# Optimization experiments

Measured on AMD Instinct MI355X. Metric: run time of the kernel, lower is better.

The kernel has to match this reference:

```python
import jax, jax.numpy as jnp
import numpy as np

NEG = -1e4      # BigBird additive mask value
LN_EPS = 1e-12  # BERT-style LayerNorm eps


def _bigbird_forward(xs_pad, mask, Wq, bq, Wk, bk, Wv, bv, Wo, bo, gamma, beta, rand_idx):
    b, n, hsz = xs_pad.shape
    H = rand_idx.shape[0]
    nb = rand_idx.shape[1] + 2          # one rand row per non-edge query block
    BS = n // nb                        # block size
    d = hsz // H
    r = rand_idx.shape[2]
    scale = 1.0 / np.sqrt(d).astype(np.float32)

    mf = mask.reshape(b, n).astype(xs_pad.dtype)   # (b,n) 1=token, 0=pad
    mb = mf.reshape(b, nb, BS)                     # blocked mask

    def proj(W, bias):
        return (xs_pad @ W + bias).reshape(b, n, H, d).transpose(0, 2, 1, 3)

    q = proj(Wq, bq) * scale            # (b,H,n,d)
    k = proj(Wk, bk)
    v = proj(Wv, bv)
    qb = q.reshape(b, H, nb, BS, d)
    kb = k.reshape(b, H, nb, BS, d)
    vb = v.reshape(b, H, nb, BS, d)

    # ---- global rows: first / last query block attend to all keys ----
    def full_row(qi):                   # qi: (b,H,BS,d)
        s = jnp.einsum('bhqd,bhkd->bhqk', qi, k) + (1.0 - mf)[:, None, None, :] * NEG
        return jnp.einsum('bhqk,bhkd->bhqd', jax.nn.softmax(s, axis=-1), v)

    ctx_first = full_row(qb[:, :, 0])
    ctx_last = full_row(qb[:, :, nb - 1])

    # ---- random key/value blocks: per-head, per-query-block gather ----
    hidx = jnp.arange(H)[:, None, None]
    rand_k = kb[:, hidx, rand_idx].reshape(b, H, nb - 2, r * BS, d)
    rand_v = vb[:, hidx, rand_idx].reshape(b, H, nb - 2, r * BS, d)
    rand_m = mb[:, rand_idx].reshape(b, H, nb - 2, r * BS)

    def sparse_row(qi, kc, vc, mc):     # kc:(b,H,K,d), mc:(b,H,K)
        s = jnp.einsum('bhqd,bhkd->bhqk', qi, kc) + (1.0 - mc)[:, :, None, :] * NEG
        return jnp.einsum('bhqk,bhkd->bhqd', jax.nn.softmax(s, axis=-1), vc)

    def gather_blocks(ids, ridx):
        kc = jnp.concatenate([kb[:, :, j] for j in ids] + [rand_k[:, :, ridx]], axis=2)
        vc = jnp.concatenate([vb[:, :, j] for j in ids] + [rand_v[:, :, ridx]], axis=2)
        mc = jnp.concatenate([jnp.broadcast_to(mb[:, None, j], (b, H, BS)) for j in ids]
                             + [rand_m[:, :, ridx]], axis=2)
        return kc, vc, mc

    # second / penultimate query blocks: window + globals + rand
    ctx_second = sparse_row(qb[:, :, 1], *gather_blocks([0, 1, 2, nb - 1], 0))
    ctx_penult = sparse_row(qb[:, :, nb - 2], *gather_blocks([nb - 3, nb - 2, nb - 1, 0], nb - 3))

    # ---- middle rows i in [2, nb-3]: 3-block sliding window + first/last global + r random ----
    nmid = nb - 4
    mid = jnp.arange(2, nb - 2)
    win = mid[:, None] + jnp.arange(-1, 2)[None, :]        # (nmid,3)
    k_win = kb[:, :, win].reshape(b, H, nmid, 3 * BS, d)
    v_win = vb[:, :, win].reshape(b, H, nmid, 3 * BS, d)
    m_win = jnp.broadcast_to(mb[:, win].reshape(b, 1, nmid, 3 * BS), (b, H, nmid, 3 * BS))

    def rep_glob(t):                     # (b,H,BS,...) -> (b,H,nmid,BS,...)
        return jnp.broadcast_to(t[:, :, None], (b, H, nmid) + t.shape[2:])

    k_mid = jnp.concatenate([k_win, rep_glob(kb[:, :, 0]), rep_glob(kb[:, :, nb - 1]),
                             rand_k[:, :, 1:nb - 3]], axis=3)
    v_mid = jnp.concatenate([v_win, rep_glob(vb[:, :, 0]), rep_glob(vb[:, :, nb - 1]),
                             rand_v[:, :, 1:nb - 3]], axis=3)
    m_first = jnp.broadcast_to(mb[:, None, None, 0], (b, H, nmid, BS))
    m_last = jnp.broadcast_to(mb[:, None, None, nb - 1], (b, H, nmid, BS))
    m_mid = jnp.concatenate([m_win, m_first, m_last, rand_m[:, :, 1:nb - 3]], axis=3)

    s_mid = jnp.einsum('bhmqd,bhmkd->bhmqk', qb[:, :, 2:nb - 2], k_mid) \
            + (1.0 - m_mid)[:, :, :, None, :] * NEG
    ctx_mid = jnp.einsum('bhmqk,bhmkd->bhmqd', jax.nn.softmax(s_mid, axis=-1), v_mid)

    ctx = jnp.concatenate([ctx_first[:, :, None], ctx_second[:, :, None], ctx_mid,
                           ctx_penult[:, :, None], ctx_last[:, :, None]], axis=2)
    ctx = ctx.reshape(b, H, n, d).transpose(0, 2, 1, 3).reshape(b, n, hsz)
    ctx = ctx * mf[:, :, None]           # from_mask on output rows

    # BigBirdSelfOutput: dense + residual + LayerNorm (dropout=0 / eval)
    y = ctx @ Wo + bo + xs_pad
    mu = y.mean(-1, keepdims=True)
    var = ((y - mu) ** 2).mean(-1, keepdims=True)
    return (y - mu) * jax.lax.rsqrt(var + LN_EPS) * gamma + beta


def setup_inputs() -> dict:
    key = jax.random.key(0)
    ks = jax.random.split(key, 6)
    B, N, HSZ, H, BS, R = 4, 4096, 1024, 16, 64, 3
    NB = N // BS
    init = lambda k, shp: jax.random.normal(k, shp, dtype=jnp.float32) * 0.02
    return {
        'xs_pad': jax.random.normal(ks[0], (B, N, HSZ), dtype=jnp.float32),
        'mask': jnp.ones((B, 1, N), dtype=jnp.int32),
        'Wq': init(ks[1], (HSZ, HSZ)), 'bq': jnp.zeros((HSZ,), jnp.float32),
        'Wk': init(ks[2], (HSZ, HSZ)), 'bk': jnp.zeros((HSZ,), jnp.float32),
        'Wv': init(ks[3], (HSZ, HSZ)), 'bv': jnp.zeros((HSZ,), jnp.float32),
        'Wo': init(ks[4], (HSZ, HSZ)), 'bo': jnp.zeros((HSZ,), jnp.float32),
        'gamma': jnp.ones((HSZ,), jnp.float32), 'beta': jnp.zeros((HSZ,), jnp.float32),
        'rand_idx': jax.random.randint(ks[5], (H, NB - 2, R), 1, NB - 1).astype(jnp.int32),
    }


def reference(xs_pad, mask, Wq, bq, Wk, bk, Wv, bv, Wo, bo, gamma, beta, rand_idx):
    return _bigbird_forward(xs_pad, mask, Wq, bq, Wk, bk, Wv, bv, Wo, bo, gamma, beta, rand_idx)
```

## Files before the change

kernel.cpp:

```cpp
#include <hip/hip_runtime.h>
#include <hip/hip_bf16.h>

#define B_   4
#define N_   4096
#define HSZ  1024
#define H_   16
#define D_   64
#define NB_  64
#define R_   3
#define M_   (B_*N_)
#define NEGV (-1e4f)
#define LOG2E 1.4426950408889634f

typedef float f32x4 __attribute__((ext_vector_type(4)));
typedef short s16x8 __attribute__((ext_vector_type(8)));
typedef __bf16 b16x8 __attribute__((ext_vector_type(8)));

__device__ __forceinline__ f32x4 mfma16(s16x8 a, s16x8 b, f32x4 c) {
  return __builtin_amdgcn_mfma_f32_16x16x32_bf16(
      __builtin_bit_cast(b16x8, a), __builtin_bit_cast(b16x8, b), c, 0, 0, 0);
}

__device__ __forceinline__ short f2b(float x) {
  __hip_bfloat16 h = __float2bfloat16(x);
  return (short)__builtin_bit_cast(unsigned short, h);
}

__device__ __forceinline__ unsigned pack2(float a, float b) {
  return (unsigned)(unsigned short)f2b(a) |
         ((unsigned)(unsigned short)f2b(b) << 16);
}

__device__ __forceinline__ void gl_lds16(const short* g, short* l) {
  __builtin_amdgcn_global_load_lds(
      (const __attribute__((address_space(1))) unsigned int*)g,
      (__attribute__((address_space(3))) unsigned int*)l, 16, 0, 0);
}

__global__ __launch_bounds__(256) void k_prep(const float* __restrict__ in,
                                              short* __restrict__ out,
                                              const float* __restrict__ Wq,
                                              const float* __restrict__ Wk,
                                              const float* __restrict__ Wv,
                                              const float* __restrict__ Wo,
                                              short* __restrict__ wt) {
  const int tid = threadIdx.x;
  if (blockIdx.x < 8192) {
    size_t i = ((size_t)blockIdx.x * 256 + tid) * 8;
    float4 a = *(const float4*)&in[i];
    float4 b = *(const float4*)&in[i + 4];
    s16x8 o;
    o[0] = f2b(a.x); o[1] = f2b(a.y); o[2] = f2b(a.z); o[3] = f2b(a.w);
    o[4] = f2b(b.x); o[5] = f2b(b.y); o[6] = f2b(b.z); o[7] = f2b(b.w);
    *(s16x8*)&out[i] = o;
    return;
  }
  const int bid = blockIdx.x - 8192;
  const int z = bid >> 8;
  const int rest = bid & 255;
  const int tk = (rest >> 4) * 64, tn = (rest & 15) * 64;
  const float* src = (z == 0) ? Wq : (z == 1) ? Wk : (z == 2) ? Wv : Wo;
  short* dst = wt + (size_t)z * HSZ * HSZ;
  __shared__ __align__(16) float t[64][68];
#pragma unroll
  for (int r = 0; r < 4; ++r) {
    int c = tid + r * 256;
    int row = c >> 4, seg = c & 15;
    *(float4*)&t[row][seg * 4] =
        *(const float4*)&src[(size_t)(tk + row) * HSZ + tn + seg * 4];
  }
  __syncthreads();
#pragma unroll
  for (int r = 0; r < 2; ++r) {
    int c = tid + r * 256;
    int row = c >> 3, seg = c & 7;
    s16x8 o;
#pragma unroll
    for (int u = 0; u < 8; ++u) o[u] = f2b(t[seg * 8 + u][row]);
    *(s16x8*)&dst[(size_t)(tn + row) * HSZ + tk + seg * 8] = o;
  }
}

template <bool SWAP>
__device__ __forceinline__ void gemm8_core(
    const short* __restrict__ A, const short* __restrict__ Bt, int tm, int tn,
    short (&a_lds)[2][256][64], short (&b_lds)[2][256][64],
    f32x4 (&acc)[8][4], int wave, int lane) {
  const int lq = lane & 15, g = lane >> 4;
  const int wm = wave >> 2, wn = wave & 3;
  const int sl8 = lane >> 3;
  const int sc = ((lane & 7) ^ sl8) * 8;

  auto ST_A = [&](int buf, int kt, int h) {
#pragma unroll
    for (int u = 0; u < 2; ++u) {
      const int rbase = h * 128 + wave * 8 + u * 64;
      gl_lds16(&A[(size_t)(tm + rbase + sl8) * HSZ + kt * 64 + sc],
               &a_lds[buf][rbase][0]);
    }
  };
  auto ST_B = [&](int buf, int kt, int h) {
#pragma unroll
    for (int u = 0; u < 2; ++u) {
      const int rbase = h * 128 + wave * 8 + u * 64;
      gl_lds16(&Bt[(size_t)(tn + rbase + sl8) * HSZ + kt * 64 + sc],
               &b_lds[buf][rbase][0]);
    }
  };

  s16x8 bf[4][2];
  auto LOADB = [&](int buf) {
#pragma unroll
    for (int j = 0; j < 4; ++j) {
      const int row = wn * 64 + j * 16 + lq;
#pragma unroll
      for (int kk = 0; kk < 2; ++kk)
        bf[j][kk] =
            *(const s16x8*)&b_lds[buf][row][((kk * 4 + g) ^ (lq & 7)) * 8];
    }
  };
  auto PH = [&](int buf, int m0) {
    s16x8 af[2][2];
#pragma unroll
    for (int i = 0; i < 2; ++i) {
      const int row = wm * 128 + (m0 + i) * 16 + lq;
#pragma unroll
      for (int kk = 0; kk < 2; ++kk)
        af[i][kk] =
            *(const s16x8*)&a_lds[buf][row][((kk * 4 + g) ^ (lq & 7)) * 8];
    }
    __builtin_amdgcn_s_setprio(1);
#pragma unroll
    for (int i = 0; i < 2; ++i)
#pragma unroll
      for (int j = 0; j < 4; ++j)
#pragma unroll
        for (int kk = 0; kk < 2; ++kk)
          acc[m0 + i][j] = SWAP
                               ? mfma16(bf[j][kk], af[i][kk], acc[m0 + i][j])
                               : mfma16(af[i][kk], bf[j][kk], acc[m0 + i][j]);
    __builtin_amdgcn_s_setprio(0);
    __builtin_amdgcn_s_barrier();
  };

  ST_A(0, 0, 0); ST_A(0, 0, 1);
  ST_B(0, 0, 0); ST_B(0, 0, 1);
  ST_B(1, 1, 0); ST_B(1, 1, 1);

  for (int p = 0; p < 8; ++p) {
    const int t = 2 * p;
    ST_A(1, t + 1, 0); ST_A(1, t + 1, 1);
    asm volatile("s_waitcnt vmcnt(8)" ::: "memory");
    __builtin_amdgcn_s_barrier();
    LOADB(0);
    PH(0, 0);
    if (t + 2 < 16) { ST_B(0, t + 2, 0); ST_B(0, t + 2, 1); }
    PH(0, 2);
    PH(0, 4);
    PH(0, 6);
    if (t + 2 < 16) { ST_A(0, t + 2, 0); ST_A(0, t + 2, 1); }
    if (p < 7) {
      asm volatile("s_waitcnt vmcnt(8)" ::: "memory");
    } else {
      asm volatile("s_waitcnt vmcnt(0)" ::: "memory");
    }
    __builtin_amdgcn_s_barrier();
    LOADB(1);
    PH(1, 0);
    if (t + 3 < 16) { ST_B(1, t + 3, 0); ST_B(1, t + 3, 1); }
    PH(1, 2);
    PH(1, 4);
    PH(1, 6);
  }
}

__global__ __launch_bounds__(512, 2) void k_qkv(
    const short* __restrict__ A, const short* __restrict__ WT,
    const float* __restrict__ bq, const float* __restrict__ bk,
    const float* __restrict__ bv, short* __restrict__ oq,
    short* __restrict__ ok, short* __restrict__ ovt) {
  const int orig = blockIdx.x;
  const int xcd = orig & 7, r = orig >> 3;
  const int tml = r / 12, rem = r % 12;
  const int z = rem >> 2, tnl = rem & 3;
  const int tm = (xcd * 8 + tml) * 256, tn = tnl * 256;
  const short* Bt = WT + (size_t)z * HSZ * HSZ;

  __shared__ __align__(16) short a_lds[2][256][64];
  __shared__ __align__(16) short b_lds[2][256][64];

  const int tid = threadIdx.x, lane = tid & 63, wave = tid >> 6;
  const int lq = lane & 15, g = lane >> 4;
  const int wm = wave >> 2, wn = wave & 3;

  f32x4 acc[8][4] = {};

  if (z == 2) {
    gemm8_core<false>(A, Bt, tm, tn, a_lds, b_lds, acc, wave, lane);
#pragma unroll
    for (int j = 0; j < 4; ++j) {
      const int col = tn + wn * 64 + j * 16 + lq;
      const int hh = col >> 6, dd = col & 63;
      const float bi = bv[col];
#pragma unroll
      for (int i = 0; i < 8; ++i) {
        const int nrow = tm + wm * 128 + i * 16 + g * 4;
        const int bb = nrow >> 12, nn = nrow & (N_ - 1);
        uint2 w;
        w.x = pack2(acc[i][j][0] + bi, acc[i][j][1] + bi);
        w.y = pack2(acc[i][j][2] + bi, acc[i][j][3] + bi);
        *(uint2*)&ovt[(((size_t)bb * H_ + hh) * D_ + dd) * N_ + nn] = w;
      }
    }
  } else {
    gemm8_core<true>(A, Bt, tm, tn, a_lds, b_lds, acc, wave, lane);
    const float* bias = z ? bk : bq;
    short* outb = z ? ok : oq;
    const float alpha = z ? 1.0f : 0.125f * LOG2E;
#pragma unroll
    for (int i = 0; i < 8; ++i) {
      const int row = tm + wm * 128 + i * 16 + lq;
#pragma unroll
      for (int j = 0; j < 4; ++j) {
        const int colb = tn + wn * 64 + j * 16 + g * 4;
        const float4 bi = *(const float4*)&bias[colb];
        const int bb = row >> 12, nn = row & (N_ - 1);
        const int hh = colb >> 6, dd = colb & 63;
        uint2 w;
        w.x = pack2((acc[i][j][0] + bi.x) * alpha,
                    (acc[i][j][1] + bi.y) * alpha);
        w.y = pack2((acc[i][j][2] + bi.z) * alpha,
                    (acc[i][j][3] + bi.w) * alpha);
        *(uint2*)&outb[(((size_t)bb * H_ + hh) * N_ + nn) * D_ + dd] = w;
      }
    }
  }
}

__global__ __launch_bounds__(512, 2) void k_out(
    const short* __restrict__ A, const short* __restrict__ WT,
    const float* __restrict__ bo, const float* __restrict__ xs,
    float* __restrict__ yout) {
  const short* Bt = WT + (size_t)3 * HSZ * HSZ;

  __shared__ __align__(16) short a_lds[2][256][64];
  __shared__ __align__(16) short b_lds[2][256][64];

  const int tid = threadIdx.x, lane = tid & 63, wave = tid >> 6;
  const int lq = lane & 15, g = lane >> 4;
  const int wm = wave >> 2, wn = wave & 3;
  const int orig = blockIdx.x;
  const int xcd = orig & 7, r = orig >> 3;
  const int tml = r >> 2, tnl = r & 3;
  const int tm = (xcd * 8 + tml) * 256, tn = tnl * 256;

  f32x4 acc[8][4] = {};
  gemm8_core<true>(A, Bt, tm, tn, a_lds, b_lds, acc, wave, lane);

#pragma unroll
  for (int i = 0; i < 8; ++i) {
    const int row = tm + wm * 128 + i * 16 + lq;
#pragma unroll
    for (int j = 0; j < 4; ++j) {
      const int colb = tn + wn * 64 + j * 16 + g * 4;
      const float4 bi = *(const float4*)&bo[colb];
      const size_t idx = (size_t)row * HSZ + colb;
      const float4 xv = *(const float4*)&xs[idx];
      float4 yv;
      yv.x = acc[i][j][0] + bi.x + xv.x;
      yv.y = acc[i][j][1] + bi.y + xv.y;
      yv.z = acc[i][j][2] + bi.z + xv.z;
      yv.w = acc[i][j][3] + bi.w + xv.w;
      *(float4*)&yout[idx] = yv;
    }
  }
}

__global__ __launch_bounds__(256) void k_attn(
    const short* __restrict__ Q, const short* __restrict__ K,
    const short* __restrict__ VT, const int* __restrict__ mask,
    const int* __restrict__ rnd, short* __restrict__ ctx,
    float* __restrict__ pO, float* __restrict__ pm, float* __restrict__ pl) {
  const int orig = blockIdx.x;
  const int swg = (orig & 7) * 624 + (orig >> 3);
  const int s = swg % 78;
  const int bh_i = swg / 78;
  const int h = bh_i & 15, b = bh_i >> 4;
  const int tid = threadIdx.x, lane = tid & 63, wave = tid >> 6;
  const int g = lane >> 4, lq = lane & 15;

  __shared__ __align__(16) short k_lds[64][64];
  __shared__ __align__(16) short vt_lds[64][64];
  __shared__ __align__(16) short p_lds[4][16][72];
  __shared__ __align__(16) float bias_s[8][64];
  __shared__ int list_s[8];
  __shared__ int Ls;

  const bool mid = (s < 62);
  const int qb = mid ? (s + 1) : (((s - 62) >> 3) ? (NB_ - 1) : 0);

  if (tid == 0) {
    int L;
    if (!mid) {
      int chunk = (s - 62) & 7;
#pragma unroll
      for (int i = 0; i < 8; ++i) list_s[i] = chunk * 8 + i;
      L = 8;
    } else {
      const int* rp = rnd + ((size_t)h * (NB_ - 2) + (qb - 1)) * R_;
      int n;
      if (qb == 1) {
        list_s[0] = 0; list_s[1] = 1; list_s[2] = 2; list_s[3] = NB_ - 1; n = 4;
      } else if (qb == NB_ - 2) {
        list_s[0] = NB_ - 3; list_s[1] = NB_ - 2; list_s[2] = NB_ - 1;
        list_s[3] = 0; n = 4;
      } else {
        list_s[0] = qb - 1; list_s[1] = qb; list_s[2] = qb + 1;
        list_s[3] = 0; list_s[4] = NB_ - 1; n = 5;
      }
      for (int j = 0; j < R_; ++j) list_s[n + j] = rp[j];
      L = n + R_;
      for (int i = L; i < 8; ++i) list_s[i] = 0;
    }
    Ls = L;
  }

  const size_t bh = (size_t)b * H_ + h;
  const size_t qrow = bh * N_ + (size_t)qb * 64 + wave * 16 + lq;
  s16x8 qf0 = *(const s16x8*)&Q[qrow * D_ + g * 8];
  s16x8 qf1 = *(const s16x8*)&Q[qrow * D_ + 32 + g * 8];

  __syncthreads();
  const int L = Ls;

  const int r0 = tid >> 3, sg = tid & 7;
  const int csl = (sg ^ (r0 & 7)) * 8;
  const int sw = (lq & 7);

  const short* Kb = K + bh * (size_t)N_ * D_;
  const short* Vb = VT + bh * (size_t)D_ * N_;
  const int* mb = mask + (size_t)b * N_;

  for (int t = tid; t < 512; t += 256) {
    const int i = t >> 6, kk2 = t & 63;
    bias_s[i][kk2] =
        (1.0f - (float)mb[list_s[i] * 64 + kk2]) * (NEGV * LOG2E);
  }

  s16x8 kr0, kr1, vr0, vr1;
  {
    const int kb = list_s[0];
    const short* kp = Kb + (size_t)kb * 64 * D_;
    const short* vp = Vb + (size_t)kb * 64;
    kr0 = *(const s16x8*)&kp[(size_t)r0 * D_ + sg * 8];
    kr1 = *(const s16x8*)&kp[(size_t)(r0 + 32) * D_ + sg * 8];
    vr0 = *(const s16x8*)&vp[(size_t)r0 * N_ + sg * 8];
    vr1 = *(const s16x8*)&vp[(size_t)(r0 + 32) * N_ + sg * 8];
  }

  s16x8 ones;
#pragma unroll
  for (int u = 0; u < 8; ++u) ones[u] = (short)0x3F80;

  f32x4 o[4] = {};
  f32x4 osum = {};
  float mshift = 0.0f;

  for (int it = 0; it < L; ++it) {
    *(s16x8*)&k_lds[r0][csl] = kr0;
    *(s16x8*)&k_lds[r0 + 32][csl] = kr1;
    *(s16x8*)&vt_lds[r0][csl] = vr0;
    *(s16x8*)&vt_lds[r0 + 32][csl] = vr1;
    if (it + 1 < L) {
      const int kb = list_s[it + 1];
      const short* kp = Kb + (size_t)kb * 64 * D_;
      const short* vp = Vb + (size_t)kb * 64;
      kr0 = *(const s16x8*)&kp[(size_t)r0 * D_ + sg * 8];
      kr1 = *(const s16x8*)&kp[(size_t)(r0 + 32) * D_ + sg * 8];
      vr0 = *(const s16x8*)&vp[(size_t)r0 * N_ + sg * 8];
      vr1 = *(const s16x8*)&vp[(size_t)(r0 + 32) * N_ + sg * 8];
    }
    __syncthreads();

    f32x4 st[4];
#pragma unroll
    for (int f = 0; f < 4; ++f) {
      f32x4 a0 = *(const f32x4*)&bias_s[it][f * 16 + g * 4];
      s16x8 af0 = *(const s16x8*)&k_lds[f * 16 + lq][(g ^ sw) * 8];
      s16x8 af1 = *(const s16x8*)&k_lds[f * 16 + lq][((4 + g) ^ sw) * 8];
      a0 = mfma16(af0, qf0, a0);
      a0 = mfma16(af1, qf1, a0);
      st[f] = a0;
    }

    if (mshift == 0.0f) {
#pragma unroll
      for (int f = 0; f < 4; ++f)
#pragma unroll
        for (int e = 0; e < 4; ++e) st[f][e] = exp2f(st[f][e]);
    } else {
#pragma unroll
      for (int f = 0; f < 4; ++f)
#pragma unroll
        for (int e = 0; e < 4; ++e) st[f][e] = exp2f(st[f][e] - mshift);
    }

#pragma unroll
    for (int f = 0; f < 4; ++f) {
      uint2 w = make_uint2(pack2(st[f][0], st[f][1]),
                           pack2(st[f][2], st[f][3]));
      *(uint2*)&p_lds[wave][lq][f * 16 + g * 4] = w;
    }

#pragma unroll
    for (int kk = 0; kk < 2; ++kk) {
      s16x8 pa = *(const s16x8*)&p_lds[wave][lq][kk * 32 + g * 8];
#pragma unroll
      for (int j = 0; j < 4; ++j) {
        s16x8 bv =
            *(const s16x8*)&vt_lds[j * 16 + lq][((kk * 4 + g) ^ sw) * 8];
        o[j] = mfma16(pa, bv, o[j]);
      }
      osum = mfma16(pa, ones, osum);
    }

    float om = fmaxf(fmaxf(osum[0], osum[1]), fmaxf(osum[2], osum[3]));
    if (__any(om > 16777216.0f)) {
#pragma unroll
      for (int j = 0; j < 4; ++j) o[j] *= 5.9604645e-08f;
      osum *= 5.9604645e-08f;
      mshift += 24.0f;
    }
    __syncthreads();
  }

  if (mid) {
    float rs[4];
#pragma unroll
    for (int e = 0; e < 4; ++e)
      rs[e] = (float)mb[qb * 64 + wave * 16 + g * 4 + e] /
              fmaxf(osum[e], 1e-30f);
#pragma unroll
    for (int j = 0; j < 4; ++j) {
      k_lds[wave * 16 + g * 4 + 0][j * 16 + lq] = f2b(o[j][0] * rs[0]);
      k_lds[wave * 16 + g * 4 + 1][j * 16 + lq] = f2b(o[j][1] * rs[1]);
      k_lds[wave * 16 + g * 4 + 2][j * 16 + lq] = f2b(o[j][2] * rs[2]);
      k_lds[wave * 16 + g * 4 + 3][j * 16 + lq] = f2b(o[j][3] * rs[3]);
    }
    __syncthreads();
#pragma unroll
    for (int pp = 0; pp < 2; ++pp) {
      int c = tid + pp * 256;
      int row = c >> 3, seg = c & 7;
      *(s16x8*)&ctx[((size_t)b * N_ + qb * 64 + row) * HSZ + h * D_ + seg * 8] =
          *(const s16x8*)&k_lds[row][seg * 8];
    }
  } else {
    const int e2 = s - 62;
    const int qsel = e2 >> 3, chunk = e2 & 7;
    const size_t eidx = (bh * 2 + qsel) * 8 + chunk;
    float* po = pO + eidx * 4096;
#pragma unroll
    for (int j = 0; j < 4; ++j)
#pragma unroll
      for (int e = 0; e < 4; ++e)
        po[(wave * 16 + g * 4 + e) * 64 + j * 16 + lq] = o[j][e];
    if (lq == 0) {
#pragma unroll
      for (int e = 0; e < 4; ++e) {
        pm[eidx * 64 + wave * 16 + g * 4 + e] = mshift;
        pl[eidx * 64 + wave * 16 + g * 4 + e] = osum[e];
      }
    }
  }
}

__global__ __launch_bounds__(256) void k_comb(
    const float* __restrict__ pO, const float* __restrict__ pm,
    const float* __restrict__ pl, const int* __restrict__ mask,
    short* __restrict__ ctx) {
  const int qsel = blockIdx.x, h = blockIdx.y, b = blockIdx.z;
  const int qb = qsel ? NB_ - 1 : 0;
  const int tid = threadIdx.x;
  const int q = tid >> 2, dq = tid & 3;
  const size_t base = (((size_t)b * H_ + h) * 2 + qsel) * 8;

  float mv[8];
  float M = -INFINITY;
#pragma unroll
  for (int i = 0; i < 8; ++i) {
    mv[i] = pm[(base + i) * 64 + q];
    M = fmaxf(M, mv[i]);
  }
  float Lsum = 0.0f;
#pragma unroll
  for (int i = 0; i < 8; ++i) {
    float w = exp2f(mv[i] - M);
    mv[i] = w;
    Lsum += pl[(base + i) * 64 + q] * w;
  }
  f32x4 acc[4] = {};
#pragma unroll
  for (int i = 0; i < 8; ++i) {
    const float* p = pO + (base + i) * 4096 + q * 64 + dq * 16;
    float w = mv[i];
#pragma unroll
    for (int u = 0; u < 4; ++u) {
      f32x4 v = *(const f32x4*)&p[u * 4];
      acc[u] += v * w;
    }
  }
  float sc = (float)mask[(size_t)b * N_ + qb * 64 + q] / fmaxf(Lsum, 1e-30f);
  s16x8 out0, out1;
#pragma unroll
  for (int u = 0; u < 8; ++u) {
    out0[u] = f2b(acc[u >> 2][u & 3] * sc);
    out1[u] = f2b(acc[2 + (u >> 2)][u & 3] * sc);
  }
  short* dst = &ctx[((size_t)b * N_ + qb * 64 + q) * HSZ + h * D_ + dq * 16];
  *(s16x8*)dst = out0;
  *(s16x8*)(dst + 8) = out1;
}

__global__ __launch_bounds__(256) void k_ln(float* __restrict__ y,
                                            const float* __restrict__ gamma,
                                            const float* __restrict__ beta) {
  const int row = blockIdx.x, tid = threadIdx.x, lane = tid & 63,
            wave = tid >> 6;
  __shared__ float s_sum[4], s_sq[4];
  float4 v = *(const float4*)&y[(size_t)row * HSZ + tid * 4];
  float s = v.x + v.y + v.z + v.w;
  float q = v.x * v.x + v.y * v.y + v.z * v.z + v.w * v.w;
#pragma unroll
  for (int m = 1; m <= 32; m <<= 1) {
    s += __shfl_xor(s, m);
    q += __shfl_xor(q, m);
  }
  if (lane == 0) { s_sum[wave] = s; s_sq[wave] = q; }
  __syncthreads();
  float S = s_sum[0] + s_sum[1] + s_sum[2] + s_sum[3];
  float Qs = s_sq[0] + s_sq[1] + s_sq[2] + s_sq[3];
  float mu = S * (1.0f / HSZ);
  float var = Qs * (1.0f / HSZ) - mu * mu;
  float r = rsqrtf(var + 1e-12f);
  float4 g = *(const float4*)&gamma[tid * 4];
  float4 be = *(const float4*)&beta[tid * 4];
  float4 outv;
  outv.x = (v.x - mu) * r * g.x + be.x;
  outv.y = (v.y - mu) * r * g.y + be.y;
  outv.z = (v.z - mu) * r * g.z + be.z;
  outv.w = (v.w - mu) * r * g.w + be.w;
  *(float4*)&y[(size_t)row * HSZ + tid * 4] = outv;
}

extern "C" void kernel_launch(void* const* d_in, const int* in_sizes, int n_in,
                              void* d_out, int out_size, void* d_ws,
                              size_t ws_size, hipStream_t stream) {
  const float* xs = (const float*)d_in[0];
  const int* mask = (const int*)d_in[1];
  const float* Wq = (const float*)d_in[2];
  const float* bq = (const float*)d_in[3];
  const float* Wk = (const float*)d_in[4];
  const float* bk = (const float*)d_in[5];
  const float* Wv = (const float*)d_in[6];
  const float* bv = (const float*)d_in[7];
  const float* Wo = (const float*)d_in[8];
  const float* bo = (const float*)d_in[9];
  const float* gamma = (const float*)d_in[10];
  const float* beta = (const float*)d_in[11];
  const int* rnd = (const int*)d_in[12];
  float* yout = (float*)d_out;

  char* ws = (char*)d_ws;
  const size_t SZ_XS = (size_t)M_ * HSZ * 2;
  const size_t SZ_WT = (size_t)4 * HSZ * HSZ * 2;
  short* xsb = (short*)ws;
  short* wt = (short*)(ws + SZ_XS);
  short* qbuf = (short*)(ws + SZ_XS + SZ_WT);
  short* kbuf = qbuf + (size_t)M_ * HSZ;
  short* vtb = kbuf + (size_t)M_ * HSZ;
  char* after = ws + SZ_XS + SZ_WT + 3 * SZ_XS;
  float* pO = (float*)(after + (1 << 20));
  float* pm = pO + (size_t)1024 * 4096;
  float* pl = pm + (size_t)1024 * 64;

  k_prep<<<9216, 256, 0, stream>>>(xs, xsb, Wq, Wk, Wv, Wo, wt);
  k_qkv<<<768, 512, 0, stream>>>(xsb, wt, bq, bk, bv, qbuf, kbuf, vtb);
  k_attn<<<4992, 256, 0, stream>>>(qbuf, kbuf, vtb, mask, rnd, xsb, pO, pm,
                                   pl);
  k_comb<<<dim3(2, H_, B_), 256, 0, stream>>>(pO, pm, pl, mask, xsb);
  k_out<<<256, 512, 0, stream>>>(xsb, wt, bo, xs, yout);
  k_ln<<<M_, 256, 0, stream>>>(yout, gamma, beta);
}
```

Before: 325.4 us.

## Double-buffer K/V tiles in attention and relax GEMM launch bounds

The attention kernel now keeps two LDS buffers for the K and V^T tiles, alternating by iteration parity. This lets it drop the trailing barrier in each key-block loop iteration, leaving one barrier per iteration instead of two. A barrier is added before the output staging that reuses buffer 0. The two GEMM kernels also drop the min-2-blocks-per-CU hint from their launch bounds, giving the compiler more register freedom at the possible cost of occupancy.

```diff
diff --git a/kernel.cpp b/kernel.cpp
--- a/kernel.cpp
+++ b/kernel.cpp
@@ -174,7 +174,7 @@
   }
 }
 
-__global__ __launch_bounds__(512, 2) void k_qkv(
+__global__ __launch_bounds__(512) void k_qkv(
     const short* __restrict__ A, const short* __restrict__ WT,
     const float* __restrict__ bq, const float* __restrict__ bk,
     const float* __restrict__ bv, short* __restrict__ oq,
@@ -237,7 +237,7 @@
   }
 }
 
-__global__ __launch_bounds__(512, 2) void k_out(
+__global__ __launch_bounds__(512) void k_out(
     const short* __restrict__ A, const short* __restrict__ WT,
     const float* __restrict__ bo, const float* __restrict__ xs,
     float* __restrict__ yout) {
@@ -289,8 +289,8 @@
   const int tid = threadIdx.x, lane = tid & 63, wave = tid >> 6;
   const int g = lane >> 4, lq = lane & 15;
 
-  __shared__ __align__(16) short k_lds[64][64];
-  __shared__ __align__(16) short vt_lds[64][64];
+  __shared__ __align__(16) short k_lds[2][64][64];
+  __shared__ __align__(16) short vt_lds[2][64][64];
   __shared__ __align__(16) short p_lds[4][16][72];
   __shared__ __align__(16) float bias_s[8][64];
   __shared__ int list_s[8];
@@ -367,10 +367,11 @@
   float mshift = 0.0f;
 
   for (int it = 0; it < L; ++it) {
-    *(s16x8*)&k_lds[r0][csl] = kr0;
-    *(s16x8*)&k_lds[r0 + 32][csl] = kr1;
-    *(s16x8*)&vt_lds[r0][csl] = vr0;
-    *(s16x8*)&vt_lds[r0 + 32][csl] = vr1;
+    const int buf = it & 1;
+    *(s16x8*)&k_lds[buf][r0][csl] = kr0;
+    *(s16x8*)&k_lds[buf][r0 + 32][csl] = kr1;
+    *(s16x8*)&vt_lds[buf][r0][csl] = vr0;
+    *(s16x8*)&vt_lds[buf][r0 + 32][csl] = vr1;
     if (it + 1 < L) {
       const int kb = list_s[it + 1];
       const short* kp = Kb + (size_t)kb * 64 * D_;
@@ -386,8 +387,8 @@
 #pragma unroll
     for (int f = 0; f < 4; ++f) {
       f32x4 a0 = *(const f32x4*)&bias_s[it][f * 16 + g * 4];
-      s16x8 af0 = *(const s16x8*)&k_lds[f * 16 + lq][(g ^ sw) * 8];
-      s16x8 af1 = *(const s16x8*)&k_lds[f * 16 + lq][((4 + g) ^ sw) * 8];
+      s16x8 af0 = *(const s16x8*)&k_lds[buf][f * 16 + lq][(g ^ sw) * 8];
+      s16x8 af1 = *(const s16x8*)&k_lds[buf][f * 16 + lq][((4 + g) ^ sw) * 8];
       a0 = mfma16(af0, qf0, a0);
       a0 = mfma16(af1, qf1, a0);
       st[f] = a0;
@@ -418,7 +419,7 @@
 #pragma unroll
       for (int j = 0; j < 4; ++j) {
         s16x8 bv =
-            *(const s16x8*)&vt_lds[j * 16 + lq][((kk * 4 + g) ^ sw) * 8];
+            *(const s16x8*)&vt_lds[buf][j * 16 + lq][((kk * 4 + g) ^ sw) * 8];
         o[j] = mfma16(pa, bv, o[j]);
       }
       osum = mfma16(pa, ones, osum);
@@ -431,7 +432,6 @@
       osum *= 5.9604645e-08f;
       mshift += 24.0f;
     }
-    __syncthreads();
   }
 
   if (mid) {
@@ -440,12 +440,14 @@
     for (int e = 0; e < 4; ++e)
       rs[e] = (float)mb[qb * 64 + wave * 16 + g * 4 + e] /
               fmaxf(osum[e], 1e-30f);
+    __syncthreads();
+    short (*ost)[64] = k_lds[0];
 #pragma unroll
     for (int j = 0; j < 4; ++j) {
-      k_lds[wave * 16 + g * 4 + 0][j * 16 + lq] = f2b(o[j][0] * rs[0]);
-      k_lds[wave * 16 + g * 4 + 1][j * 16 + lq] = f2b(o[j][1] * rs[1]);
-      k_lds[wave * 16 + g * 4 + 2][j * 16 + lq] = f2b(o[j][2] * rs[2]);
-      k_lds[wave * 16 + g * 4 + 3][j * 16 + lq] = f2b(o[j][3] * rs[3]);
+      ost[wave * 16 + g * 4 + 0][j * 16 + lq] = f2b(o[j][0] * rs[0]);
+      ost[wave * 16 + g * 4 + 1][j * 16 + lq] = f2b(o[j][1] * rs[1]);
+      ost[wave * 16 + g * 4 + 2][j * 16 + lq] = f2b(o[j][2] * rs[2]);
+      ost[wave * 16 + g * 4 + 3][j * 16 + lq] = f2b(o[j][3] * rs[3]);
     }
     __syncthreads();
 #pragma unroll
@@ -453,7 +455,7 @@
       int c = tid + pp * 256;
       int row = c >> 3, seg = c & 7;
       *(s16x8*)&ctx[((size_t)b * N_ + qb * 64 + row) * HSZ + h * D_ + seg * 8] =
-          *(const s16x8*)&k_lds[row][seg * 8];
+          *(const s16x8*)&ost[row][seg * 8];
     }
   } else {
     const int e2 = s - 62;
```

New measurement: 323.6 us. No clear change (-0.5%).
